# Performance work log

Measured on AMD Instinct MI355X. Metric: run time of the kernel, lower is better.

## Reference

```python
import jax, jax.numpy as jnp
import numpy as np

SCALE = 0.5

def setup_inputs() -> dict:
    key = jax.random.key(0)
    kx, kw, kb = jax.random.split(key, 3)
    N, Cin, H, W = 32, 64, 128, 128
    Cout, K = 128, 3
    x = jax.random.normal(kx, (N, Cin, H, W), dtype=jnp.float32)
    # kaiming_uniform with a=sqrt(5) -> bound = sqrt(3/fan_in) approx; uniform is fine for a reference
    fan_in = Cin * K * K
    bound = 1.0 / np.sqrt(fan_in)
    weight = jax.random.uniform(kw, (Cout, Cin, K, K), dtype=jnp.float32, minval=-bound, maxval=bound)
    bias = jax.random.uniform(kb, (Cout,), dtype=jnp.float32, minval=-bound, maxval=bound)
    return {"x": x, "weight": weight, "bias": bias}

def reference(x, weight, bias):
    # valid conv, stride 1: (N, Cout, OH, OW)
    y = jax.lax.conv_general_dilated(
        x, weight,
        window_strides=(1, 1),
        padding="VALID",
        dimension_numbers=("NCHW", "OIHW", "NCHW"),
    )
    y = (y + bias[None, :, None, None]) * SCALE
    # min over output channels, keepdim -> (N, 1, OH, OW)
    return jnp.min(y, axis=1, keepdims=True)
```

## Files before the change

### kernel.cpp

```cpp
#include <hip/hip_runtime.h>
#include <hip/hip_bf16.h>

constexpr int CN   = 32;
constexpr int CIN  = 64;
constexpr int CH   = 128;
constexpr int CW   = 128;
constexpr int COUT = 128;
constexpr int OHh  = 126;
constexpr int OWw  = 126;
constexpr int KTOT = 576;

typedef __attribute__((ext_vector_type(8))) short bf16x8;
typedef __attribute__((ext_vector_type(4))) float f32x4;

__device__ __forceinline__ unsigned short f2bf(float f) {
  union { float f; unsigned u; } v; v.f = f;
  unsigned u = v.u;
  u += 0x7FFFu + ((u >> 16) & 1u);
  return (unsigned short)(u >> 16);
}

__device__ __forceinline__ unsigned packbf2(float a, float b) {
  union { __hip_bfloat162 h; unsigned u; } v;
  v.h = __float22bfloat162_rn(make_float2(a, b));
  return v.u;
}

__global__ void prep_wt3_kernel(const float* __restrict__ w,
                                unsigned short* __restrict__ wt3) {
  int e = blockIdx.x * 256 + threadIdx.x;
  if (e >= COUT * KTOT) return;
  int j = e & 7, lane = (e >> 3) & 63, mi = (e >> 9) & 3, wc = (e >> 11) & 1;
  int p = e >> 12;
  int G = p / 3, kw = p - G * 3;
  int kh = G >> 1, half = G & 1;
  int co = wc * 64 + mi * 16 + (lane & 15);
  int ci = half * 32 + (lane >> 4) * 8 + j;
  wt3[e] = f2bf(w[co * 576 + ci * 9 + kh * 3 + kw]);
}

__global__ __launch_bounds__(256, 4)
void conv_min_mfma9(const float* __restrict__ x,
                    const unsigned short* __restrict__ wt3,
                    const float* __restrict__ bias,
                    float* __restrict__ out) {
  __shared__ __align__(16) unsigned short sX[2][130][32];
  __shared__ float sRed[2][128];

  const int t   = threadIdx.x;
  const int bid = blockIdx.x;
  const int swz = (bid & 7) * 504 + (bid >> 3);
  const int n   = swz / OHh;
  const int oh  = swz - n * OHh;

  const int lane = t & 63, w = t >> 6;
  const int wc = w & 1;
  const int wp = w >> 1;
  const int lg = lane >> 4, ln = lane & 15;

  const int sc = t & 127;
  const int o0 = (t >> 7) * 2;

  int Bb[3];
  #pragma unroll
  for (int kw = 0; kw < 3; ++kw) {
    int row = wp * 64 + ln + kw;
    int ch = lg ^ ((row >> 1) & 3);
    Bb[kw] = row * 64 + ch * 16;
  }
  const unsigned short* wlane = wt3 + wc * 2048 + lane * 8;

  f32x4 acc[4][4];
  #pragma unroll
  for (int i = 0; i < 4; ++i)
    #pragma unroll
    for (int j = 0; j < 4; ++j)
      acc[i][j] = (f32x4){0.f, 0.f, 0.f, 0.f};

  float sv[2][8];

  auto loadX = [&](int G) {
    const int h = oh + (G >> 1);
    #pragma unroll
    for (int r = 0; r < 2; ++r) {
      const size_t base =
          ((size_t)((n * 64 + (G & 1) * 32 + (o0 + r) * 8) * 128 + h)) * 128 + sc;
      #pragma unroll
      for (int j = 0; j < 8; ++j)
        sv[r][j] = x[base + (size_t)j * 16384];
    }
  };
  auto writeX = [&](int dbuf) {
    #pragma unroll
    for (int r = 0; r < 2; ++r) {
      const int ch = (o0 + r) ^ ((sc >> 1) & 3);
      uint4 v = make_uint4(packbf2(sv[r][0], sv[r][1]), packbf2(sv[r][2], sv[r][3]),
                           packbf2(sv[r][4], sv[r][5]), packbf2(sv[r][6], sv[r][7]));
      *(uint4*)(&sX[dbuf][sc][ch * 8]) = v;
    }
  };

  loadX(0);
  writeX(0);
  asm volatile("s_waitcnt lgkmcnt(0)" ::: "memory");
  __builtin_amdgcn_s_barrier();
  __builtin_amdgcn_sched_barrier(0);

  #pragma unroll
  for (int p = 0; p < 18; ++p) {
    const int G = p / 3, kw = p - G * 3, dbuf = G & 1;

    if (kw == 0 && G < 5)
      loadX(G + 1);

    bf16x8 bfr[4];
    #pragma unroll
    for (int ni = 0; ni < 4; ++ni)
      bfr[ni] = *(const bf16x8*)((const char*)&sX[0][0][0] +
                                 dbuf * 8320 + Bb[kw] + ni * 1024);
    __builtin_amdgcn_s_setprio(1);
    #pragma unroll
    for (int mi = 0; mi < 4; ++mi) {
      bf16x8 af = *(const bf16x8*)(wlane + p * 4096 + mi * 512);
      #pragma unroll
      for (int ni = 0; ni < 4; ++ni)
        acc[mi][ni] = __builtin_amdgcn_mfma_f32_16x16x32_bf16(
            af, bfr[ni], acc[mi][ni], 0, 0, 0);
    }
    __builtin_amdgcn_s_setprio(0);

    if (kw == 2 && G < 5) {
      writeX(dbuf ^ 1);
      asm volatile("s_waitcnt lgkmcnt(0)" ::: "memory");
      __builtin_amdgcn_s_barrier();
      __builtin_amdgcn_sched_barrier(0);
    }
  }

  float bv[4][4];
  #pragma unroll
  for (int mi = 0; mi < 4; ++mi)
    #pragma unroll
    for (int r = 0; r < 4; ++r)
      bv[mi][r] = bias[wc * 64 + mi * 16 + lg * 4 + r];

  #pragma unroll
  for (int ni = 0; ni < 4; ++ni) {
    float m = 3.4e38f;
    #pragma unroll
    for (int mi = 0; mi < 4; ++mi)
      #pragma unroll
      for (int r = 0; r < 4; ++r)
        m = fminf(m, (acc[mi][ni][r] + bv[mi][r]) * 0.5f);
    m = fminf(m, __shfl_xor(m, 16));
    m = fminf(m, __shfl_xor(m, 32));
    if (lg == 0) sRed[wc][wp * 64 + ni * 16 + ln] = m;
  }
  __syncthreads();
  if (t < OWw)
    out[((size_t)n * OHh + oh) * OWw + t] = fminf(sRed[0][t], sRed[1][t]);
}

__global__ __launch_bounds__(256, 2)
void conv_min_fb(const float* __restrict__ x, const float* __restrict__ w,
                 const float* __restrict__ bias, float* __restrict__ out) {
  __shared__ __align__(16) unsigned short sW[128][40];
  __shared__ __align__(16) unsigned short sX[128][40];
  __shared__ float sBias[COUT];
  __shared__ float sRed[2][128];
  const int t = threadIdx.x, bid = blockIdx.x;
  const int n = bid / OHh, oh = bid - n * OHh;
  if (t < COUT) sBias[t] = bias[t];
  const int hq = t & 7, q = t >> 3, c0 = q * 4;
  const int wco = t >> 1, whalf = t & 1;
  const int lane = t & 63, lg = lane >> 4, ln = lane & 15;
  const int wv = t >> 6, wc = wv & 1, wp = wv >> 1;
  f32x4 acc[4][4];
  #pragma unroll
  for (int i = 0; i < 4; ++i)
    #pragma unroll
    for (int j = 0; j < 4; ++j) acc[i][j] = (f32x4){0.f, 0.f, 0.f, 0.f};
  const float* xn = x + (size_t)n * CIN * CH * CW;
  for (int s = 0; s < 18; ++s) {
    const int kw_s = s / 6;
    const int rembase = (s - kw_s * 6) * 32;
    float4 xa[2], xb[2]; int kkp[2];
    #pragma unroll
    for (int pi = 0; pi < 2; ++pi) {
      const int kk = 2 * hq + 16 * pi; kkp[pi] = kk;
      int rem0 = rembase + kk, ci0 = rem0 / 3, kh0 = rem0 - ci0 * 3;
      int rem1 = rem0 + 1, ci1 = rem1 / 3, kh1 = rem1 - ci1 * 3;
      xa[pi] = *(const float4*)(xn + (ci0 * CH + (oh + kh0)) * CW + c0);
      xb[pi] = *(const float4*)(xn + (ci1 * CH + (oh + kh1)) * CW + c0);
    }
    unsigned tmp[8];
    #pragma unroll
    for (int e = 0; e < 8; ++e) {
      int kk = whalf * 16 + 2 * e;
      int rem0 = rembase + kk, ci0 = rem0 / 3, kh0 = rem0 - ci0 * 3;
      int rem1 = rem0 + 1, ci1 = rem1 / 3, kh1 = rem1 - ci1 * 3;
      tmp[e] = (unsigned)f2bf(w[wco * 576 + ci0 * 9 + kh0 * 3 + kw_s]) |
               ((unsigned)f2bf(w[wco * 576 + ci1 * 9 + kh1 * 3 + kw_s]) << 16);
    }
    __syncthreads();
    #pragma unroll
    for (int pi = 0; pi < 2; ++pi)
      #pragma unroll
      for (int j = 0; j < 4; ++j) {
        int p = c0 + j - kw_s;
        unsigned pk = (unsigned)f2bf(((const float*)&xa[pi])[j]) |
                      ((unsigned)f2bf(((const float*)&xb[pi])[j]) << 16);
        if (p >= 0) *(unsigned*)&sX[p][kkp[pi]] = pk;
      }
    *(uint4*)&sW[wco][whalf * 16] = make_uint4(tmp[0], tmp[1], tmp[2], tmp[3]);
    *(uint4*)&sW[wco][whalf * 16 + 8] = make_uint4(tmp[4], tmp[5], tmp[6], tmp[7]);
    __syncthreads();
    bf16x8 af[4], bfr[4];
    #pragma unroll
    for (int mi = 0; mi < 4; ++mi) af[mi] = *(const bf16x8*)&sW[wc * 64 + mi * 16 + ln][lg * 8];
    #pragma unroll
    for (int ni = 0; ni < 4; ++ni) bfr[ni] = *(const bf16x8*)&sX[wp * 64 + ni * 16 + ln][lg * 8];
    #pragma unroll
    for (int mi = 0; mi < 4; ++mi)
      #pragma unroll
      for (int ni = 0; ni < 4; ++ni)
        acc[mi][ni] = __builtin_amdgcn_mfma_f32_16x16x32_bf16(af[mi], bfr[ni], acc[mi][ni], 0, 0, 0);
  }
  #pragma unroll
  for (int ni = 0; ni < 4; ++ni) {
    float m = 3.4e38f;
    #pragma unroll
    for (int mi = 0; mi < 4; ++mi)
      #pragma unroll
      for (int r = 0; r < 4; ++r)
        m = fminf(m, (acc[mi][ni][r] + sBias[wc * 64 + mi * 16 + lg * 4 + r]) * 0.5f);
    m = fminf(m, __shfl_xor(m, 16));
    m = fminf(m, __shfl_xor(m, 32));
    if (lg == 0) sRed[wc][wp * 64 + ni * 16 + ln] = m;
  }
  __syncthreads();
  if (t < OWw) out[(size_t)(n * OHh + oh) * OWw + t] = fminf(sRed[0][t], sRed[1][t]);
}

extern "C" void kernel_launch(void* const* d_in, const int* in_sizes, int n_in,
                              void* d_out, int out_size, void* d_ws, size_t ws_size,
                              hipStream_t stream) {
  const float* x    = (const float*)d_in[0];
  const float* w    = (const float*)d_in[1];
  const float* bias = (const float*)d_in[2];
  float* out = (float*)d_out;

  const size_t WT_BYTES = (size_t)COUT * KTOT * 2;

  if (d_ws && ws_size >= WT_BYTES) {
    unsigned short* wt3 = (unsigned short*)d_ws;
    prep_wt3_kernel<<<(COUT * KTOT + 255) / 256, 256, 0, stream>>>(w, wt3);
    conv_min_mfma9<<<CN * OHh, 256, 0, stream>>>(x, wt3, bias, out);
  } else {
    conv_min_fb<<<CN * OHh, 256, 0, stream>>>(x, w, bias, out);
  }
}
```

Baseline: 92.86 us.

## Compute two output rows per block to reuse weight fragments across rows

Each block now produces two adjacent output rows instead of one. Each wave covers one row at full width with 8 N-tiles, so every weight A-fragment loaded from global memory feeds twice as many MFMAs. The grid is halved, the LDS staging buffer and accumulators double, and launch bounds drop to 2 blocks per CU. This cuts weight reloads and per-block overhead at the cost of higher register pressure and lower occupancy.

```diff
diff --git a/kernel.cpp b/kernel.cpp
--- a/kernel.cpp
+++ b/kernel.cpp
@@ -39,23 +39,23 @@
   wt3[e] = f2bf(w[co * 576 + ci * 9 + kh * 3 + kw]);
 }
 
-__global__ __launch_bounds__(256, 4)
-void conv_min_mfma9(const float* __restrict__ x,
-                    const unsigned short* __restrict__ wt3,
-                    const float* __restrict__ bias,
-                    float* __restrict__ out) {
-  __shared__ __align__(16) unsigned short sX[2][130][32];
-  __shared__ float sRed[2][128];
+__global__ __launch_bounds__(256, 2)
+void conv_min_mfma10(const float* __restrict__ x,
+                     const unsigned short* __restrict__ wt3,
+                     const float* __restrict__ bias,
+                     float* __restrict__ out) {
+  __shared__ __align__(16) unsigned short sX[2][2][130][32];
+  __shared__ float sRed[2][256];
 
   const int t   = threadIdx.x;
   const int bid = blockIdx.x;
-  const int swz = (bid & 7) * 504 + (bid >> 3);
-  const int n   = swz / OHh;
-  const int oh  = swz - n * OHh;
+  const int swz = (bid & 7) * 252 + (bid >> 3);
+  const int n   = swz / 63;
+  const int oh0 = (swz - n * 63) * 2;
 
   const int lane = t & 63, w = t >> 6;
   const int wc = w & 1;
-  const int wp = w >> 1;
+  const int wr = w >> 1;
   const int lg = lane >> 4, ln = lane & 15;
 
   const int sc = t & 127;
@@ -64,40 +64,47 @@
   int Bb[3];
   #pragma unroll
   for (int kw = 0; kw < 3; ++kw) {
-    int row = wp * 64 + ln + kw;
+    int row = ln + kw;
     int ch = lg ^ ((row >> 1) & 3);
-    Bb[kw] = row * 64 + ch * 16;
+    Bb[kw] = wr * 8320 + row * 64 + ch * 16;
   }
   const unsigned short* wlane = wt3 + wc * 2048 + lane * 8;
 
-  f32x4 acc[4][4];
+  f32x4 acc[4][8];
   #pragma unroll
   for (int i = 0; i < 4; ++i)
     #pragma unroll
-    for (int j = 0; j < 4; ++j)
+    for (int j = 0; j < 8; ++j)
       acc[i][j] = (f32x4){0.f, 0.f, 0.f, 0.f};
 
-  float sv[2][8];
+  float sv[2][2][8];
 
   auto loadX = [&](int G) {
-    const int h = oh + (G >> 1);
     #pragma unroll
     for (int r = 0; r < 2; ++r) {
-      const size_t base =
-          ((size_t)((n * 64 + (G & 1) * 32 + (o0 + r) * 8) * 128 + h)) * 128 + sc;
-      #pragma unroll
-      for (int j = 0; j < 8; ++j)
-        sv[r][j] = x[base + (size_t)j * 16384];
+      const int h = oh0 + r + (G >> 1);
+      #pragma unroll
+      for (int k = 0; k < 2; ++k) {
+        const size_t base =
+            ((size_t)((n * 64 + (G & 1) * 32 + (o0 + k) * 8) * 128 + h)) * 128 + sc;
+        #pragma unroll
+        for (int j = 0; j < 8; ++j)
+          sv[r][k][j] = x[base + (size_t)j * 16384];
+      }
     }
   };
   auto writeX = [&](int dbuf) {
     #pragma unroll
-    for (int r = 0; r < 2; ++r) {
-      const int ch = (o0 + r) ^ ((sc >> 1) & 3);
-      uint4 v = make_uint4(packbf2(sv[r][0], sv[r][1]), packbf2(sv[r][2], sv[r][3]),
-                           packbf2(sv[r][4], sv[r][5]), packbf2(sv[r][6], sv[r][7]));
-      *(uint4*)(&sX[dbuf][sc][ch * 8]) = v;
-    }
+    for (int r = 0; r < 2; ++r)
+      #pragma unroll
+      for (int k = 0; k < 2; ++k) {
+        const int ch = (o0 + k) ^ ((sc >> 1) & 3);
+        uint4 v = make_uint4(packbf2(sv[r][k][0], sv[r][k][1]),
+                             packbf2(sv[r][k][2], sv[r][k][3]),
+                             packbf2(sv[r][k][4], sv[r][k][5]),
+                             packbf2(sv[r][k][6], sv[r][k][7]));
+        *(uint4*)(&sX[dbuf][r][sc][ch * 8]) = v;
+      }
   };
 
   loadX(0);
@@ -113,17 +120,17 @@
     if (kw == 0 && G < 5)
       loadX(G + 1);
 
-    bf16x8 bfr[4];
-    #pragma unroll
-    for (int ni = 0; ni < 4; ++ni)
-      bfr[ni] = *(const bf16x8*)((const char*)&sX[0][0][0] +
-                                 dbuf * 8320 + Bb[kw] + ni * 1024);
+    bf16x8 bfr[8];
+    #pragma unroll
+    for (int ni = 0; ni < 8; ++ni)
+      bfr[ni] = *(const bf16x8*)((const char*)&sX[0][0][0][0] +
+                                 dbuf * 16640 + Bb[kw] + ni * 1024);
     __builtin_amdgcn_s_setprio(1);
     #pragma unroll
     for (int mi = 0; mi < 4; ++mi) {
       bf16x8 af = *(const bf16x8*)(wlane + p * 4096 + mi * 512);
       #pragma unroll
-      for (int ni = 0; ni < 4; ++ni)
+      for (int ni = 0; ni < 8; ++ni)
         acc[mi][ni] = __builtin_amdgcn_mfma_f32_16x16x32_bf16(
             af, bfr[ni], acc[mi][ni], 0, 0, 0);
     }
@@ -145,7 +152,7 @@
       bv[mi][r] = bias[wc * 64 + mi * 16 + lg * 4 + r];
 
   #pragma unroll
-  for (int ni = 0; ni < 4; ++ni) {
+  for (int ni = 0; ni < 8; ++ni) {
     float m = 3.4e38f;
     #pragma unroll
     for (int mi = 0; mi < 4; ++mi)
@@ -154,11 +161,14 @@
         m = fminf(m, (acc[mi][ni][r] + bv[mi][r]) * 0.5f);
     m = fminf(m, __shfl_xor(m, 16));
     m = fminf(m, __shfl_xor(m, 32));
-    if (lg == 0) sRed[wc][wp * 64 + ni * 16 + ln] = m;
+    if (lg == 0) sRed[wc][wr * 128 + ni * 16 + ln] = m;
   }
   __syncthreads();
-  if (t < OWw)
-    out[((size_t)n * OHh + oh) * OWw + t] = fminf(sRed[0][t], sRed[1][t]);
+  {
+    int row = t >> 7, c = t & 127;
+    if (c < OWw)
+      out[((size_t)n * OHh + oh0 + row) * OWw + c] = fminf(sRed[0][t], sRed[1][t]);
+  }
 }
 
 __global__ __launch_bounds__(256, 2)
@@ -255,7 +265,7 @@
   if (d_ws && ws_size >= WT_BYTES) {
     unsigned short* wt3 = (unsigned short*)d_ws;
     prep_wt3_kernel<<<(COUT * KTOT + 255) / 256, 256, 0, stream>>>(w, wt3);
-    conv_min_mfma9<<<CN * OHh, 256, 0, stream>>>(x, wt3, bias, out);
+    conv_min_mfma10<<<2016, 256, 0, stream>>>(x, wt3, bias, out);
   } else {
     conv_min_fb<<<CN * OHh, 256, 0, stream>>>(x, w, bias, out);
   }
```

Measured after the change: 238.9 us. 157% more time.

## Pre-transpose input to channel-last bf16 and stream it with direct-to-LDS loads

Applied to the files above, without the earlier changes.

Adds a prep kernel that converts x to bf16 in a per-row channel-last, swizzled layout. The main conv kernel then fills shared memory with global_load_lds DMA instead of strided fp32 loads plus conversion and LDS writes. Each wave now covers all 128 output channels for 32 columns, so the cross-wave min reduction through shared memory goes away. B fragments are double-buffered in registers. The cost is an extra full pass over x (read fp32, write bf16 of about 67MB) plus a larger workspace requirement.

```diff
diff --git a/kernel.cpp b/kernel.cpp
--- a/kernel.cpp
+++ b/kernel.cpp
@@ -1,5 +1,4 @@
 #include <hip/hip_runtime.h>
-#include <hip/hip_bf16.h>
 
 constexpr int CN   = 32;
 constexpr int CIN  = 64;
@@ -20,32 +19,61 @@
   return (unsigned short)(u >> 16);
 }
 
-__device__ __forceinline__ unsigned packbf2(float a, float b) {
-  union { __hip_bfloat162 h; unsigned u; } v;
-  v.h = __float22bfloat162_rn(make_float2(a, b));
-  return v.u;
-}
-
-__global__ void prep_wt3_kernel(const float* __restrict__ w,
-                                unsigned short* __restrict__ wt3) {
+__device__ __forceinline__ void gload_lds16(const unsigned short* g, unsigned short* l) {
+  __builtin_amdgcn_global_load_lds(
+      (const __attribute__((address_space(1))) unsigned int*)g,
+      (__attribute__((address_space(3))) unsigned int*)l, 16, 0, 0);
+}
+
+__global__ __launch_bounds__(256) void prep_xt_kernel(const float* __restrict__ x,
+                                                      unsigned short* __restrict__ xt) {
+  __shared__ __align__(16) unsigned short s[128][72];
+  const int b = blockIdx.x;
+  const int n = b >> 7, h = b & 127;
+  const float* src = x + (size_t)n * CIN * CH * CW + (size_t)h * CW;
+  const int t = threadIdx.x;
+  #pragma unroll
+  for (int r = 0; r < 8; ++r) {
+    int idx = r * 256 + t;
+    int ci = idx >> 5, c0 = (idx & 31) << 2;
+    float4 v = *(const float4*)(src + (size_t)ci * (CH * CW) + c0);
+    s[c0 + 0][ci] = f2bf(v.x);
+    s[c0 + 1][ci] = f2bf(v.y);
+    s[c0 + 2][ci] = f2bf(v.z);
+    s[c0 + 3][ci] = f2bf(v.w);
+  }
+  __syncthreads();
+  unsigned short* dst = xt + (size_t)b * 8192;
+  #pragma unroll
+  for (int r = 0; r < 4; ++r) {
+    int idx = r * 256 + t;
+    int c = idx >> 3, sl = idx & 7;
+    int half = sl >> 2, q = sl & 3;
+    int lo = q ^ ((c >> 1) & 3);
+    uint4 v = *(const uint4*)&s[c][half * 32 + lo * 8];
+    *(uint4*)(dst + (size_t)c * 64 + sl * 8) = v;
+  }
+}
+
+__global__ void prep_wt4_kernel(const float* __restrict__ w,
+                                unsigned short* __restrict__ wt4) {
   int e = blockIdx.x * 256 + threadIdx.x;
   if (e >= COUT * KTOT) return;
-  int j = e & 7, lane = (e >> 3) & 63, mi = (e >> 9) & 3, wc = (e >> 11) & 1;
+  int j = e & 7, lane = (e >> 3) & 63, mi = (e >> 9) & 7;
   int p = e >> 12;
   int G = p / 3, kw = p - G * 3;
   int kh = G >> 1, half = G & 1;
-  int co = wc * 64 + mi * 16 + (lane & 15);
+  int co = mi * 16 + (lane & 15);
   int ci = half * 32 + (lane >> 4) * 8 + j;
-  wt3[e] = f2bf(w[co * 576 + ci * 9 + kh * 3 + kw]);
+  wt4[e] = f2bf(w[co * 576 + ci * 9 + kh * 3 + kw]);
 }
 
 __global__ __launch_bounds__(256, 4)
-void conv_min_mfma9(const float* __restrict__ x,
-                    const unsigned short* __restrict__ wt3,
-                    const float* __restrict__ bias,
-                    float* __restrict__ out) {
-  __shared__ __align__(16) unsigned short sX[2][130][32];
-  __shared__ float sRed[2][128];
+void conv_min_mfma12(const unsigned short* __restrict__ xt,
+                     const unsigned short* __restrict__ wt4,
+                     const float* __restrict__ bias,
+                     float* __restrict__ out) {
+  __shared__ __align__(16) unsigned short sX[2][132][32];
 
   const int t   = threadIdx.x;
   const int bid = blockIdx.x;
@@ -54,111 +82,93 @@
   const int oh  = swz - n * OHh;
 
   const int lane = t & 63, w = t >> 6;
-  const int wc = w & 1;
-  const int wp = w >> 1;
   const int lg = lane >> 4, ln = lane & 15;
 
-  const int sc = t & 127;
-  const int o0 = (t >> 7) * 2;
+  const int seg0 = w * 2;
+  const int cA = seg0 * 16 + (lane >> 2);
+  const int srcA = cA * 64 + (lane & 3) * 8;
+  const int srcB = srcA + 16 * 64;
 
   int Bb[3];
   #pragma unroll
   for (int kw = 0; kw < 3; ++kw) {
-    int row = wp * 64 + ln + kw;
+    int row = w * 32 + ln + kw;
     int ch = lg ^ ((row >> 1) & 3);
     Bb[kw] = row * 64 + ch * 16;
   }
-  const unsigned short* wlane = wt3 + wc * 2048 + lane * 8;
-
-  f32x4 acc[4][4];
-  #pragma unroll
-  for (int i = 0; i < 4; ++i)
-    #pragma unroll
-    for (int j = 0; j < 4; ++j)
+  const unsigned short* wlane = wt4 + lane * 8;
+
+  f32x4 acc[8][2];
+  #pragma unroll
+  for (int i = 0; i < 8; ++i)
+    #pragma unroll
+    for (int j = 0; j < 2; ++j)
       acc[i][j] = (f32x4){0.f, 0.f, 0.f, 0.f};
 
-  float sv[2][8];
-
-  auto loadX = [&](int G) {
+  bf16x8 bfr[2][2];
+
+  auto stage = [&](int G, int buf) {
     const int h = oh + (G >> 1);
-    #pragma unroll
-    for (int r = 0; r < 2; ++r) {
-      const size_t base =
-          ((size_t)((n * 64 + (G & 1) * 32 + (o0 + r) * 8) * 128 + h)) * 128 + sc;
-      #pragma unroll
-      for (int j = 0; j < 8; ++j)
-        sv[r][j] = x[base + (size_t)j * 16384];
-    }
+    const size_t base = (size_t)(n * 128 + h) * 8192 + (G & 1) * 32;
+    unsigned short* dst = &sX[buf][0][0] + seg0 * 512;
+    gload_lds16(xt + base + srcA, dst);
+    gload_lds16(xt + base + srcB, dst + 512);
   };
-  auto writeX = [&](int dbuf) {
-    #pragma unroll
-    for (int r = 0; r < 2; ++r) {
-      const int ch = (o0 + r) ^ ((sc >> 1) & 3);
-      uint4 v = make_uint4(packbf2(sv[r][0], sv[r][1]), packbf2(sv[r][2], sv[r][3]),
-                           packbf2(sv[r][4], sv[r][5]), packbf2(sv[r][6], sv[r][7]));
-      *(uint4*)(&sX[dbuf][sc][ch * 8]) = v;
-    }
+  auto ldB = [&](int p, int slot) {
+    const int G = p / 3, kw = p - G * 3, buf = G & 1;
+    #pragma unroll
+    for (int ni = 0; ni < 2; ++ni)
+      bfr[slot][ni] = *(const bf16x8*)((const char*)&sX[0][0][0] +
+                                       buf * 8448 + Bb[kw] + ni * 1024);
   };
 
-  loadX(0);
-  writeX(0);
-  asm volatile("s_waitcnt lgkmcnt(0)" ::: "memory");
+  if (t < 128) {
+    int buf = t >> 6, i = t & 63;
+    ((unsigned*)&sX[buf][128][0])[i] = 0u;
+  }
+  stage(0, 0);
+  asm volatile("s_waitcnt vmcnt(0) lgkmcnt(0)" ::: "memory");
   __builtin_amdgcn_s_barrier();
   __builtin_amdgcn_sched_barrier(0);
+  ldB(0, 0);
 
   #pragma unroll
   for (int p = 0; p < 18; ++p) {
-    const int G = p / 3, kw = p - G * 3, dbuf = G & 1;
-
-    if (kw == 0 && G < 5)
-      loadX(G + 1);
-
-    bf16x8 bfr[4];
-    #pragma unroll
-    for (int ni = 0; ni < 4; ++ni)
-      bfr[ni] = *(const bf16x8*)((const char*)&sX[0][0][0] +
-                                 dbuf * 8320 + Bb[kw] + ni * 1024);
+    const int G = p / 3, kw = p - G * 3, cur = p & 1;
+    if (kw == 0 && G < 5) stage(G + 1, (G & 1) ^ 1);
+    if (kw < 2) ldB(p + 1, cur ^ 1);
     __builtin_amdgcn_s_setprio(1);
     #pragma unroll
-    for (int mi = 0; mi < 4; ++mi) {
-      bf16x8 af = *(const bf16x8*)(wlane + p * 4096 + mi * 512);
-      #pragma unroll
-      for (int ni = 0; ni < 4; ++ni)
+    for (int mi = 0; mi < 8; ++mi) {
+      bf16x8 af = *(const bf16x8*)(wlane + (p * 8 + mi) * 512);
+      #pragma unroll
+      for (int ni = 0; ni < 2; ++ni)
         acc[mi][ni] = __builtin_amdgcn_mfma_f32_16x16x32_bf16(
-            af, bfr[ni], acc[mi][ni], 0, 0, 0);
+            af, bfr[cur][ni], acc[mi][ni], 0, 0, 0);
     }
     __builtin_amdgcn_s_setprio(0);
-
     if (kw == 2 && G < 5) {
-      writeX(dbuf ^ 1);
-      asm volatile("s_waitcnt lgkmcnt(0)" ::: "memory");
+      asm volatile("s_waitcnt vmcnt(0)" ::: "memory");
       __builtin_amdgcn_s_barrier();
       __builtin_amdgcn_sched_barrier(0);
-    }
-  }
-
-  float bv[4][4];
-  #pragma unroll
-  for (int mi = 0; mi < 4; ++mi)
-    #pragma unroll
-    for (int r = 0; r < 4; ++r)
-      bv[mi][r] = bias[wc * 64 + mi * 16 + lg * 4 + r];
-
-  #pragma unroll
-  for (int ni = 0; ni < 4; ++ni) {
+      ldB(p + 1, cur ^ 1);
+    }
+  }
+
+  #pragma unroll
+  for (int ni = 0; ni < 2; ++ni) {
     float m = 3.4e38f;
     #pragma unroll
-    for (int mi = 0; mi < 4; ++mi)
+    for (int mi = 0; mi < 8; ++mi)
       #pragma unroll
       for (int r = 0; r < 4; ++r)
-        m = fminf(m, (acc[mi][ni][r] + bv[mi][r]) * 0.5f);
+        m = fminf(m, (acc[mi][ni][r] + bias[mi * 16 + lg * 4 + r]) * 0.5f);
     m = fminf(m, __shfl_xor(m, 16));
     m = fminf(m, __shfl_xor(m, 32));
-    if (lg == 0) sRed[wc][wp * 64 + ni * 16 + ln] = m;
-  }
-  __syncthreads();
-  if (t < OWw)
-    out[((size_t)n * OHh + oh) * OWw + t] = fminf(sRed[0][t], sRed[1][t]);
+    int col = w * 32 + ni * 16 + ln;
+    if (lg == 0 && col < OWw)
+      out[((size_t)n * OHh + oh) * OWw + col] = m;
+  }
 }
 
 __global__ __launch_bounds__(256, 2)
@@ -250,12 +260,15 @@
   const float* bias = (const float*)d_in[2];
   float* out = (float*)d_out;
 
+  const size_t XT_BYTES = (size_t)CN * CH * CW * CIN * 2;
   const size_t WT_BYTES = (size_t)COUT * KTOT * 2;
 
-  if (d_ws && ws_size >= WT_BYTES) {
-    unsigned short* wt3 = (unsigned short*)d_ws;
-    prep_wt3_kernel<<<(COUT * KTOT + 255) / 256, 256, 0, stream>>>(w, wt3);
-    conv_min_mfma9<<<CN * OHh, 256, 0, stream>>>(x, wt3, bias, out);
+  if (d_ws && ws_size >= XT_BYTES + WT_BYTES) {
+    unsigned short* xt  = (unsigned short*)d_ws;
+    unsigned short* wt4 = (unsigned short*)((char*)d_ws + XT_BYTES);
+    prep_xt_kernel<<<CN * CH, 256, 0, stream>>>(x, xt);
+    prep_wt4_kernel<<<(COUT * KTOT + 255) / 256, 256, 0, stream>>>(w, wt4);
+    conv_min_mfma12<<<CN * OHh, 256, 0, stream>>>(xt, wt4, bias, out);
   } else {
     conv_min_fb<<<CN * OHh, 256, 0, stream>>>(x, w, bias, out);
   }
```

Result: slower. 126.5 us (+36.2%).

## Compute two output rows per block with each wave covering all output channels

Applied to the files above, without the earlier changes.

Each block now produces two adjacent output rows instead of one. Each wave computes all 128 output channels for one row and a 64-column half, so the channel-min finishes inside the wave and the shared-memory cross-wave reduction and its final barrier go away. Each weight fragment is reused across twice as many pixels, while the input rows shared between the two output rows are staged in one pass. In exchange the accumulator count per thread doubles, so launch bounds drop to 2 blocks per CU, which raises register pressure and lowers occupancy. The shared-memory padding columns are zeroed to cover reads past column 127.

```diff
diff --git a/kernel.cpp b/kernel.cpp
--- a/kernel.cpp
+++ b/kernel.cpp
@@ -26,80 +26,84 @@
   return v.u;
 }
 
-__global__ void prep_wt3_kernel(const float* __restrict__ w,
-                                unsigned short* __restrict__ wt3) {
+__global__ void prep_wt4_kernel(const float* __restrict__ w,
+                                unsigned short* __restrict__ wt4) {
   int e = blockIdx.x * 256 + threadIdx.x;
   if (e >= COUT * KTOT) return;
-  int j = e & 7, lane = (e >> 3) & 63, mi = (e >> 9) & 3, wc = (e >> 11) & 1;
+  int j = e & 7, lane = (e >> 3) & 63, mi = (e >> 9) & 7;
   int p = e >> 12;
   int G = p / 3, kw = p - G * 3;
   int kh = G >> 1, half = G & 1;
-  int co = wc * 64 + mi * 16 + (lane & 15);
+  int co = mi * 16 + (lane & 15);
   int ci = half * 32 + (lane >> 4) * 8 + j;
-  wt3[e] = f2bf(w[co * 576 + ci * 9 + kh * 3 + kw]);
-}
-
-__global__ __launch_bounds__(256, 4)
-void conv_min_mfma9(const float* __restrict__ x,
-                    const unsigned short* __restrict__ wt3,
-                    const float* __restrict__ bias,
-                    float* __restrict__ out) {
-  __shared__ __align__(16) unsigned short sX[2][130][32];
-  __shared__ float sRed[2][128];
+  wt4[e] = f2bf(w[co * 576 + ci * 9 + kh * 3 + kw]);
+}
+
+__global__ __launch_bounds__(256, 2)
+void conv_min_mfma13(const float* __restrict__ x,
+                     const unsigned short* __restrict__ wt4,
+                     const float* __restrict__ bias,
+                     float* __restrict__ out) {
+  __shared__ __align__(16) unsigned short sX[2][2][132][32];
 
   const int t   = threadIdx.x;
   const int bid = blockIdx.x;
-  const int swz = (bid & 7) * 504 + (bid >> 3);
-  const int n   = swz / OHh;
-  const int oh  = swz - n * OHh;
+  const int swz = (bid & 7) * 252 + (bid >> 3);
+  const int n   = swz / 63;
+  const int oh0 = (swz - n * 63) * 2;
 
   const int lane = t & 63, w = t >> 6;
-  const int wc = w & 1;
-  const int wp = w >> 1;
+  const int wr = w >> 1;
+  const int wh = w & 1;
   const int lg = lane >> 4, ln = lane & 15;
 
-  const int sc = t & 127;
-  const int o0 = (t >> 7) * 2;
+  const int rs = t >> 7;
+  const int cs = t & 127;
 
   int Bb[3];
   #pragma unroll
   for (int kw = 0; kw < 3; ++kw) {
-    int row = wp * 64 + ln + kw;
-    int ch = lg ^ ((row >> 1) & 3);
-    Bb[kw] = row * 64 + ch * 16;
-  }
-  const unsigned short* wlane = wt3 + wc * 2048 + lane * 8;
-
-  f32x4 acc[4][4];
-  #pragma unroll
-  for (int i = 0; i < 4; ++i)
+    int c0 = wh * 64 + ln + kw;
+    int ch = lg ^ ((c0 >> 1) & 3);
+    Bb[kw] = wr * 8448 + c0 * 64 + ch * 16;
+  }
+  const unsigned short* wlane = wt4 + lane * 8;
+
+  f32x4 acc[8][4];
+  #pragma unroll
+  for (int i = 0; i < 8; ++i)
     #pragma unroll
     for (int j = 0; j < 4; ++j)
       acc[i][j] = (f32x4){0.f, 0.f, 0.f, 0.f};
 
-  float sv[2][8];
+  float sv[4][8];
 
   auto loadX = [&](int G) {
-    const int h = oh + (G >> 1);
-    #pragma unroll
-    for (int r = 0; r < 2; ++r) {
+    const int h = oh0 + rs + (G >> 1);
+    #pragma unroll
+    for (int o = 0; o < 4; ++o) {
       const size_t base =
-          ((size_t)((n * 64 + (G & 1) * 32 + (o0 + r) * 8) * 128 + h)) * 128 + sc;
+          ((size_t)((n * 64 + (G & 1) * 32 + o * 8) * 128 + h)) * 128 + cs;
       #pragma unroll
       for (int j = 0; j < 8; ++j)
-        sv[r][j] = x[base + (size_t)j * 16384];
+        sv[o][j] = x[base + (size_t)j * 16384];
     }
   };
-  auto writeX = [&](int dbuf) {
-    #pragma unroll
-    for (int r = 0; r < 2; ++r) {
-      const int ch = (o0 + r) ^ ((sc >> 1) & 3);
-      uint4 v = make_uint4(packbf2(sv[r][0], sv[r][1]), packbf2(sv[r][2], sv[r][3]),
-                           packbf2(sv[r][4], sv[r][5]), packbf2(sv[r][6], sv[r][7]));
-      *(uint4*)(&sX[dbuf][sc][ch * 8]) = v;
+  auto writeX = [&](int buf) {
+    char* dst = (char*)&sX[0][0][0][0] + buf * 16896 + rs * 8448 + cs * 64;
+    #pragma unroll
+    for (int o = 0; o < 4; ++o) {
+      const int ch = o ^ ((cs >> 1) & 3);
+      uint4 v = make_uint4(packbf2(sv[o][0], sv[o][1]), packbf2(sv[o][2], sv[o][3]),
+                           packbf2(sv[o][4], sv[o][5]), packbf2(sv[o][6], sv[o][7]));
+      *(uint4*)(dst + ch * 16) = v;
     }
   };
 
+  {
+    int buf = t >> 7, r = (t >> 6) & 1, i = t & 63;
+    *((unsigned*)((char*)&sX[0][0][0][0] + buf * 16896 + r * 8448 + 128 * 64) + i) = 0u;
+  }
   loadX(0);
   writeX(0);
   asm volatile("s_waitcnt lgkmcnt(0)" ::: "memory");
@@ -108,20 +112,22 @@
 
   #pragma unroll
   for (int p = 0; p < 18; ++p) {
-    const int G = p / 3, kw = p - G * 3, dbuf = G & 1;
-
-    if (kw == 0 && G < 5)
+    const int G = p / 3, kw = p - G * 3, buf = G & 1;
+
+    if (kw == 0 && G < 5) {
       loadX(G + 1);
+      __builtin_amdgcn_sched_barrier(0);
+    }
 
     bf16x8 bfr[4];
     #pragma unroll
     for (int ni = 0; ni < 4; ++ni)
-      bfr[ni] = *(const bf16x8*)((const char*)&sX[0][0][0] +
-                                 dbuf * 8320 + Bb[kw] + ni * 1024);
+      bfr[ni] = *(const bf16x8*)((const char*)&sX[0][0][0][0] +
+                                 buf * 16896 + Bb[kw] + ni * 1024);
     __builtin_amdgcn_s_setprio(1);
     #pragma unroll
-    for (int mi = 0; mi < 4; ++mi) {
-      bf16x8 af = *(const bf16x8*)(wlane + p * 4096 + mi * 512);
+    for (int mi = 0; mi < 8; ++mi) {
+      bf16x8 af = *(const bf16x8*)(wlane + (p * 8 + mi) * 512);
       #pragma unroll
       for (int ni = 0; ni < 4; ++ni)
         acc[mi][ni] = __builtin_amdgcn_mfma_f32_16x16x32_bf16(
@@ -130,35 +136,27 @@
     __builtin_amdgcn_s_setprio(0);
 
     if (kw == 2 && G < 5) {
-      writeX(dbuf ^ 1);
+      writeX(buf ^ 1);
       asm volatile("s_waitcnt lgkmcnt(0)" ::: "memory");
       __builtin_amdgcn_s_barrier();
       __builtin_amdgcn_sched_barrier(0);
     }
   }
 
-  float bv[4][4];
-  #pragma unroll
-  for (int mi = 0; mi < 4; ++mi)
-    #pragma unroll
-    for (int r = 0; r < 4; ++r)
-      bv[mi][r] = bias[wc * 64 + mi * 16 + lg * 4 + r];
-
   #pragma unroll
   for (int ni = 0; ni < 4; ++ni) {
     float m = 3.4e38f;
     #pragma unroll
-    for (int mi = 0; mi < 4; ++mi)
+    for (int mi = 0; mi < 8; ++mi)
       #pragma unroll
       for (int r = 0; r < 4; ++r)
-        m = fminf(m, (acc[mi][ni][r] + bv[mi][r]) * 0.5f);
+        m = fminf(m, (acc[mi][ni][r] + bias[mi * 16 + lg * 4 + r]) * 0.5f);
     m = fminf(m, __shfl_xor(m, 16));
     m = fminf(m, __shfl_xor(m, 32));
-    if (lg == 0) sRed[wc][wp * 64 + ni * 16 + ln] = m;
-  }
-  __syncthreads();
-  if (t < OWw)
-    out[((size_t)n * OHh + oh) * OWw + t] = fminf(sRed[0][t], sRed[1][t]);
+    int col = wh * 64 + ni * 16 + ln;
+    if (lg == 0 && col < OWw)
+      out[((size_t)n * OHh + oh0 + wr) * OWw + col] = m;
+  }
 }
 
 __global__ __launch_bounds__(256, 2)
@@ -253,9 +251,9 @@
   const size_t WT_BYTES = (size_t)COUT * KTOT * 2;
 
   if (d_ws && ws_size >= WT_BYTES) {
-    unsigned short* wt3 = (unsigned short*)d_ws;
-    prep_wt3_kernel<<<(COUT * KTOT + 255) / 256, 256, 0, stream>>>(w, wt3);
-    conv_min_mfma9<<<CN * OHh, 256, 0, stream>>>(x, wt3, bias, out);
+    unsigned short* wt4 = (unsigned short*)d_ws;
+    prep_wt4_kernel<<<(COUT * KTOT + 255) / 256, 256, 0, stream>>>(w, wt4);
+    conv_min_mfma13<<<2016, 256, 0, stream>>>(x, wt4, bias, out);
   } else {
     conv_min_fb<<<CN * OHh, 256, 0, stream>>>(x, w, bias, out);
   }
```

Result: slower. 118.3 us (+27.4%).
